# Kernel optimization log

Measured on AMD Instinct MI355X. Metric: run time of the kernel, lower is better.

The kernel has to match this reference:

```python
import jax, jax.numpy as jnp
import numpy as np

B, S, D, H, L = 32, 512, 256, 8, 3
HD = D // H
FFN = D // 2
SCALE_BASE = 512.0
EPS = 1e-5


def _gammas():
    return (1.0 - jnp.exp(jnp.linspace(np.log(1.0 / 32.0), np.log(1.0 / 512.0), H))).astype(jnp.float32)


def _xpos(x, downscale):
    # x: [..., S, hd]; XPOS rotary embedding with exponential length scaling
    s, hd = x.shape[-2], x.shape[-1]
    half = hd // 2
    scale = (jnp.arange(0, hd, 2, dtype=jnp.float32) + 0.4 * hd) / (1.4 * hd)  # [half]
    power = jnp.arange(s, dtype=jnp.float32)[:, None] / SCALE_BASE
    sm = scale[None, :] ** power  # [S, half]
    if downscale:
        sm = 1.0 / sm
    inv_freq = 1.0 / (10000.0 ** (jnp.arange(half, dtype=jnp.float32) / half))
    ang = jnp.arange(s, dtype=jnp.float32)[:, None] * inv_freq[None, :]  # [S, half]
    sin = jnp.repeat(jnp.sin(ang) * sm, 2, axis=-1)  # duplicate_interleave -> [S, hd]
    cos = jnp.repeat(jnp.cos(ang) * sm, 2, axis=-1)
    x1, x2 = x[..., ::2], x[..., 1::2]
    rot = jnp.stack((-x2, x1), axis=-1).reshape(x.shape)  # rotate_every_two
    return x * cos + rot * sin


def _layer_norm(x, w, b):
    mu = x.mean(-1, keepdims=True)
    var = ((x - mu) ** 2).mean(-1, keepdims=True)
    return (x - mu) / jnp.sqrt(var + EPS) * w + b


def _msr(X, WQ, WK, WV, WG, WO, gn_w, gn_b):
    # Multi-scale retention, parallel form. X: [B,S,D]; WQ/WK/WV: [H,D,HD]
    b, s, _ = X.shape
    Q = _xpos(jnp.einsum('bsd,hde->bhse', X, WQ), False)
    K = _xpos(jnp.einsum('bsd,hde->bhse', X, WK), True)
    V = jnp.einsum('bsd,hde->bhse', X, WV)
    n = jnp.arange(s)
    delta = (n[:, None] - n[None, :]).astype(jnp.float32)
    mask = n[:, None] >= n[None, :]
    g = _gammas()
    Dm = jnp.where(mask[None], g[:, None, None] ** delta[None], 0.0)  # [H,S,S]
    scores = jnp.einsum('bhse,bhte->bhst', Q, K) * Dm[None]  # [B,H,S,S]
    Y = jnp.einsum('bhst,bhte->bhse', scores, V)  # [B,H,S,HD]
    Y = jnp.moveaxis(Y, 1, 2)  # [B,S,H,HD] (= concat heads)
    # GroupNorm(heads, v_dim): normalize per (token, head) group
    mu = Y.mean(-1, keepdims=True)
    var = ((Y - mu) ** 2).mean(-1, keepdims=True)
    Yn = ((Y - mu) / jnp.sqrt(var + EPS)).reshape(b, s, D) * gn_w + gn_b
    G = X @ WG
    return (G * jax.nn.sigmoid(G) * Yn) @ WO


def setup_inputs() -> dict:
    key = jax.random.key(0)
    ks = jax.random.split(key, 10)
    inp = {
        'v': jax.random.randint(ks[0], (B, S), 0, 65, dtype=jnp.int64),
        'emb': jax.random.normal(ks[1], (65, D), dtype=jnp.float32),
        'WQ': jax.random.normal(ks[2], (L, H, D, HD), dtype=jnp.float32) / D,
        'WK': jax.random.normal(ks[3], (L, H, D, HD), dtype=jnp.float32) / D,
        'WV': jax.random.normal(ks[4], (L, H, D, HD), dtype=jnp.float32) / D,
        'WG': jax.random.normal(ks[5], (L, D, D), dtype=jnp.float32) / D,
        'WO': jax.random.normal(ks[6], (L, D, D), dtype=jnp.float32) / D,
        'gn_w': jnp.ones((L, D), jnp.float32),
        'gn_b': jnp.zeros((L, D), jnp.float32),
        'ln1_w': jnp.ones((L, D), jnp.float32),
        'ln1_b': jnp.zeros((L, D), jnp.float32),
        'ln2_w': jnp.ones((L, D), jnp.float32),
        'ln2_b': jnp.zeros((L, D), jnp.float32),
        'w1': jax.random.normal(ks[7], (L, D, FFN), dtype=jnp.float32) * (1.0 / np.sqrt(D)),
        'b1': jnp.zeros((L, FFN), jnp.float32),
        'w2': jax.random.normal(ks[8], (L, FFN, D), dtype=jnp.float32) * (1.0 / np.sqrt(FFN)),
        'b2': jnp.zeros((L, D), jnp.float32),
    }
    return inp


def reference(v, emb, WQ, WK, WV, WG, WO, gn_w, gn_b, ln1_w, ln1_b, ln2_w, ln2_b, w1, b1, w2, b2):
    emb = emb.at[0].set(0.0)  # padding_idx=0
    X = jax.nn.relu(emb[v])  # [B,S,D]
    for i in range(L):
        Y = _msr(_layer_norm(X, ln1_w[i], ln1_b[i]), WQ[i], WK[i], WV[i], WG[i], WO[i], gn_w[i], gn_b[i]) + X
        h = jax.nn.gelu(_layer_norm(Y, ln2_w[i], ln2_b[i]) @ w1[i] + b1[i], approximate=False)
        X = h @ w2[i] + b2[i] + Y
    return X
```

## Files before the change

kernel.cpp:

```cpp
#include <hip/hip_runtime.h>
#include <hip/hip_bf16.h>
#include <math.h>

#define BB 32
#define SS 512
#define DD 256
#define HH 8
#define HDIM 32
#define FFNN 128
#define NROWS (BB*SS)
#define NELEM (NROWS*DD)

using bf16 = __hip_bfloat16;
typedef __attribute__((ext_vector_type(8))) short short8;
typedef __attribute__((ext_vector_type(4))) short short4v;
typedef __attribute__((ext_vector_type(4))) float floatx4;
typedef unsigned int uint_al __attribute__((may_alias));

static __device__ __forceinline__ float bf2f(bf16 x) { return __bfloat162float(x); }
static __device__ __forceinline__ bf16  f2bf(float x) { return __float2bfloat16(x); }
static __device__ __forceinline__ short f2bfs(float x) {
    bf16 b = __float2bfloat16(x);
    return __builtin_bit_cast(short, b);
}

static __device__ __forceinline__ unsigned int cvtpk(float a, float b) {
    unsigned int r;
    asm("v_cvt_pk_bf16_f32 %0, %1, %2" : "=v"(r) : "v"(a), "v"(b));
    return r;
}
static __device__ __forceinline__ short4v mk4(unsigned int a, unsigned int b) {
    union { unsigned int u[2]; short4v s; } t;
    t.u[0] = a; t.u[1] = b;
    return t.s;
}
static __device__ __forceinline__ floatx4 mfma16(short4v a, short4v b, floatx4 c) {
#if __has_builtin(__builtin_amdgcn_mfma_f32_16x16x16bf16_1k)
    return __builtin_amdgcn_mfma_f32_16x16x16bf16_1k(a, b, c, 0, 0, 0);
#else
    asm("v_mfma_f32_16x16x16_bf16 %0, %1, %2, %0" : "+v"(c) : "v"(a), "v"(b));
    return c;
#endif
}

static __device__ __forceinline__ void gld_lds16(const void* g, void* l) {
    __builtin_amdgcn_global_load_lds(
        (const __attribute__((address_space(1))) void*)g,
        (__attribute__((address_space(3))) void*)l, 16, 0, 0);
}

__global__ __launch_bounds__(256) void detect_v(const int* __restrict__ v, int* __restrict__ flag) {
    int i = blockIdx.x * 256 + threadIdx.x;
    if (v[2 * i + 1] != 0) atomicOr(flag, 1);
}

#define NQKVG (3*1024*256)
#define NWO   (3*256*256)
#define NW1   (3*128*256)
#define NW2   (3*256*128)
#define NXPT  (512*16)
#define NSETUP (NQKVG+NWO+NW1+NW2+NXPT)
__global__ __launch_bounds__(256) void setup_pack(const float* __restrict__ WQ, const float* __restrict__ WK,
                                                  const float* __restrict__ WV, const float* __restrict__ WG,
                                                  const float* __restrict__ WO, const float* __restrict__ w1,
                                                  const float* __restrict__ w2,
                                                  bf16* __restrict__ dQ, bf16* __restrict__ dO,
                                                  bf16* __restrict__ d1, bf16* __restrict__ d2,
                                                  float4* __restrict__ xpt, int* __restrict__ flag) {
    int idx = blockIdx.x * 256 + threadIdx.x;
    if (idx == 0) *flag = 0;
    if (idx < NQKVG) {
        int k = idx & 255, n = (idx >> 8) & 1023, l = idx >> 18;
        int seg = n >> 8, n8 = n & 255;
        float val;
        if (seg < 3) {
            const float* W = (seg == 0) ? WQ : (seg == 1) ? WK : WV;
            int h = n8 >> 5, e = n8 & 31;
            val = W[(((size_t)l * 8 + h) * 256 + k) * 32 + e];
        } else {
            val = WG[(size_t)l * 65536 + k * 256 + n8];
        }
        dQ[((size_t)l * 1024 + n) * 256 + k] = f2bf(val);
    } else if (idx < NQKVG + NWO) {
        int i = idx - NQKVG;
        int k = i & 255, n = (i >> 8) & 255, l = i >> 16;
        dO[((size_t)l * 256 + n) * 256 + k] = f2bf(WO[(size_t)l * 65536 + k * 256 + n]);
    } else if (idx < NQKVG + NWO + NW1) {
        int i = idx - NQKVG - NWO;
        int k = i & 255, n = (i >> 8) & 127, l = i >> 15;
        d1[((size_t)l * 128 + n) * 256 + k] = f2bf(w1[(size_t)l * 32768 + k * 128 + n]);
    } else if (idx < NQKVG + NWO + NW1 + NW2) {
        int i = idx - NQKVG - NWO - NW1;
        int k = i & 127, n = (i >> 7) & 255, l = i >> 15;
        d2[((size_t)l * 256 + n) * 128 + k] = f2bf(w2[(size_t)l * 32768 + k * 256 + n]);
    } else {
        int i = idx - NQKVG - NWO - NW1 - NW2;
        int jf = i & 15, s = i >> 4;
        float base = (2.0f * jf + 12.8f) / 44.8f;
        float sm = powf(base, (float)s * (1.0f / 512.0f));
        float ang = (float)s * powf(10000.0f, -(float)jf / 16.0f);
        float sn, cs;
        sincosf(ang, &sn, &cs);
        xpt[i] = float4{cs * sm, sn * sm, cs / sm, sn / sm};
    }
}

__global__ __launch_bounds__(256) void embed_ln_kernel(const int* __restrict__ v,
                                                       const float* __restrict__ emb,
                                                       const int* __restrict__ flag,
                                                       const float* __restrict__ w,
                                                       const float* __restrict__ b,
                                                       float* __restrict__ X,
                                                       short* __restrict__ Xn) {
    __shared__ float p1[4], p2[4], st[2];
    const int d = threadIdx.x;
    const int wid = threadIdx.x >> 6;
    const int is32 = *flag;
    const float wd = w[d], bd = b[d];
    for (int it = 0; it < 8; ++it) {
        int row = blockIdx.x * 8 + it;
        int tok = is32 ? v[row] : v[2 * row];
        float x = 0.0f;
        if (tok != 0) {
            x = emb[tok * DD + d];
            x = x > 0.0f ? x : 0.0f;
        }
        X[(size_t)row * DD + d] = x;
        float s1 = x, s2 = x * x;
        #pragma unroll
        for (int off = 1; off < 64; off <<= 1) {
            s1 += __shfl_xor(s1, off);
            s2 += __shfl_xor(s2, off);
        }
        if ((threadIdx.x & 63) == 0) { p1[wid] = s1; p2[wid] = s2; }
        __syncthreads();
        if (threadIdx.x == 0) {
            float t1 = p1[0] + p1[1] + p1[2] + p1[3];
            float t2 = p2[0] + p2[1] + p2[2] + p2[3];
            float mu = t1 * (1.0f / DD);
            float var = t2 * (1.0f / DD) - mu * mu;
            st[0] = mu; st[1] = rsqrtf(var + 1e-5f);
        }
        __syncthreads();
        Xn[(size_t)row * DD + d] = f2bfs((x - st[0]) * st[1] * wd + bd);
    }
}

__global__ __launch_bounds__(256) void qkvg_gemm(const short* __restrict__ A,
                                                 const short* __restrict__ Bp,
                                                 const float4* __restrict__ xpt,
                                                 bf16* __restrict__ C) {
    __shared__ __align__(16) short Als[16 * 512];
    __shared__ __align__(16) short Bls[16 * 512];
    const int tid = threadIdx.x;
    const int wave = tid >> 6, lane = tid & 63, lo = lane & 15, quad = lane >> 4;
    const int wm = wave >> 1, wn = wave & 1;
    const int row0 = blockIdx.x * 128, col0 = blockIdx.y * 128;

    floatx4 acc[4][4];
    #pragma unroll
    for (int i = 0; i < 4; ++i)
        #pragma unroll
        for (int j = 0; j < 4; ++j) acc[i][j] = floatx4{0.f, 0.f, 0.f, 0.f};

    for (int k0 = 0; k0 < 256; k0 += 64) {
        #pragma unroll
        for (int t = 0; t < 4; ++t) {
            int grp = (wm * 4 + t) * 2 + wn;
            const short* ga = A + (size_t)(row0 + (wm * 4 + t) * 16 + lo) * 256
                            + k0 + (wn * 4 + quad) * 8;
            gld_lds16(ga, &Als[grp * 512]);
        }
        #pragma unroll
        for (int t = 0; t < 4; ++t) {
            int grp = (wn * 4 + t) * 2 + wm;
            const short* gb = Bp + (size_t)(col0 + (wn * 4 + t) * 16 + lo) * 256
                            + k0 + (wm * 4 + quad) * 8;
            gld_lds16(gb, &Bls[grp * 512]);
        }
        __syncthreads();
        #pragma unroll
        for (int kkgrp = 0; kkgrp < 2; ++kkgrp) {
            short8 af[4], bfr[4];
            #pragma unroll
            for (int t = 0; t < 4; ++t)
                af[t] = *(const short8*)(&Als[((wm * 4 + t) * 2 + kkgrp) * 512 + lane * 8]);
            #pragma unroll
            for (int t = 0; t < 4; ++t)
                bfr[t] = *(const short8*)(&Bls[((wn * 4 + t) * 2 + kkgrp) * 512 + lane * 8]);
            #pragma unroll
            for (int ti = 0; ti < 4; ++ti)
                #pragma unroll
                for (int tj = 0; tj < 4; ++tj)
                    acc[ti][tj] = __builtin_amdgcn_mfma_f32_16x16x32_bf16(af[ti], bfr[tj], acc[ti][tj], 0, 0, 0);
        }
        __syncthreads();
    }

    #pragma unroll
    for (int ti = 0; ti < 4; ++ti) {
        #pragma unroll
        for (int tj = 0; tj < 4; ++tj) {
            int colb = col0 + (wn * 4 + tj) * 16 + lo;
            int seg = colb >> 8;
            #pragma unroll
            for (int r = 0; r < 4; ++r) {
                int row = row0 + (wm * 4 + ti) * 16 + quad * 4 + r;
                float v = acc[ti][tj][r];
                if (seg < 2) {
                    int s = row & (SS - 1);
                    int jf = (colb & 31) >> 1;
                    float4 t = xpt[s * 16 + jf];
                    float cs = (seg == 0) ? t.x : t.z;
                    float sn = (seg == 0) ? t.y : t.w;
                    float p = __shfl_xor(v, 1);
                    v = (lo & 1) ? (v * cs + p * sn) : (v * cs - p * sn);
                }
                C[(size_t)row * 1024 + colb] = f2bf(v);
            }
        }
    }
}

#define HS2 264
#define HSTR 136
template<int DOLN>
__global__ __launch_bounds__(256) void wo_ffn_fused(const short* __restrict__ A,
                                                    const short* __restrict__ Wo,
                                                    const short* __restrict__ W1p,
                                                    const float* __restrict__ b1,
                                                    const short* __restrict__ W2p,
                                                    const float* __restrict__ b2,
                                                    float* __restrict__ X,
                                                    const float* __restrict__ ln2w,
                                                    const float* __restrict__ ln2b,
                                                    const float* __restrict__ ln1w,
                                                    const float* __restrict__ ln1b,
                                                    short* __restrict__ Xn) {
    __shared__ __align__(16) short Als[4 * 512];
    __shared__ __align__(16) short Bls[4][8 * 512];
    __shared__ __align__(16) short Hn[32 * HS2];
    __shared__ __align__(16) short Hf[32 * HSTR];
    __shared__ float Ssum[32][4], Ssq[32][4];
    const int tid = threadIdx.x;
    const int wave = tid >> 6, lane = tid & 63, lo = lane & 15, quad = lane >> 4;
    const int row0 = blockIdx.x * 32;
    const int colw0 = wave * 64;

    floatx4 acc[2][4];
    #pragma unroll
    for (int i = 0; i < 2; ++i)
        #pragma unroll
        for (int j = 0; j < 4; ++j) acc[i][j] = floatx4{0.f, 0.f, 0.f, 0.f};

    const short* Ab = A + (size_t)(row0 + (wave >> 1) * 16 + lo) * 1024 + ((wave & 1) * 4 + quad) * 8;
    const short* Bb = Wo + (size_t)(colw0 + lo) * 256 + quad * 8;

    for (int k0 = 0; k0 < 256; k0 += 64) {
        gld_lds16(Ab + k0, &Als[wave * 512]);
        #pragma unroll
        for (int t = 0; t < 4; ++t)
            #pragma unroll
            for (int kk = 0; kk < 2; ++kk)
                gld_lds16(Bb + (size_t)(t * 16) * 256 + k0 + kk * 32,
                          &Bls[wave][(t * 2 + kk) * 512]);
        __syncthreads();
        #pragma unroll
        for (int kk = 0; kk < 2; ++kk) {
            short8 af[2], bfr[4];
            #pragma unroll
            for (int t = 0; t < 2; ++t)
                af[t] = *(const short8*)(&Als[(t * 2 + kk) * 512 + lane * 8]);
            #pragma unroll
            for (int t = 0; t < 4; ++t)
                bfr[t] = *(const short8*)(&Bls[wave][(t * 2 + kk) * 512 + lane * 8]);
            #pragma unroll
            for (int ti = 0; ti < 2; ++ti)
                #pragma unroll
                for (int tj = 0; tj < 4; ++tj)
                    acc[ti][tj] = __builtin_amdgcn_mfma_f32_16x16x32_bf16(af[ti], bfr[tj], acc[ti][tj], 0, 0, 0);
        }
        __syncthreads();
    }

    float vv[2][4][4];
    #pragma unroll
    for (int ti = 0; ti < 2; ++ti)
        #pragma unroll
        for (int tj = 0; tj < 4; ++tj) {
            int colb = colw0 + tj * 16 + lo;
            #pragma unroll
            for (int r = 0; r < 4; ++r) {
                int row = row0 + ti * 16 + quad * 4 + r;
                vv[ti][tj][r] = acc[ti][tj][r] + X[(size_t)row * DD + colb];
            }
        }
    #pragma unroll
    for (int ti = 0; ti < 2; ++ti)
        #pragma unroll
        for (int r = 0; r < 4; ++r) {
            float s1 = 0.f, s2 = 0.f;
            #pragma unroll
            for (int tj = 0; tj < 4; ++tj) {
                float v = vv[ti][tj][r];
                s1 += v; s2 += v * v;
            }
            #pragma unroll
            for (int off = 1; off < 16; off <<= 1) {
                s1 += __shfl_xor(s1, off);
                s2 += __shfl_xor(s2, off);
            }
            if (lo == 0) {
                int rl = ti * 16 + quad * 4 + r;
                Ssum[rl][wave] = s1;
                Ssq[rl][wave] = s2;
            }
        }
    __syncthreads();
    #pragma unroll
    for (int ti = 0; ti < 2; ++ti)
        #pragma unroll
        for (int r = 0; r < 4; ++r) {
            int rl = ti * 16 + quad * 4 + r;
            float t1 = Ssum[rl][0] + Ssum[rl][1] + Ssum[rl][2] + Ssum[rl][3];
            float t2 = Ssq[rl][0] + Ssq[rl][1] + Ssq[rl][2] + Ssq[rl][3];
            float mu = t1 * (1.0f / DD);
            float var = t2 * (1.0f / DD) - mu * mu;
            float rs = rsqrtf(var + 1e-5f);
            #pragma unroll
            for (int tj = 0; tj < 4; ++tj) {
                int colb = colw0 + tj * 16 + lo;
                Hn[rl * HS2 + colb] =
                    f2bfs((vv[ti][tj][r] - mu) * rs * ln2w[colb] + ln2b[colb]);
            }
        }
    __syncthreads();

    floatx4 a1[2][2];
    #pragma unroll
    for (int i = 0; i < 2; ++i) { a1[i][0] = floatx4{0,0,0,0}; a1[i][1] = floatx4{0,0,0,0}; }
    const short* Bb1 = W1p + (size_t)(wave * 32 + lo) * 256 + quad * 8;
    for (int k0 = 0; k0 < 256; k0 += 64) {
        #pragma unroll
        for (int t = 0; t < 2; ++t)
            #pragma unroll
            for (int kk = 0; kk < 2; ++kk)
                gld_lds16(Bb1 + (size_t)(t * 16) * 256 + k0 + kk * 32,
                          &Bls[wave][(t * 2 + kk) * 512]);
        __syncthreads();
        #pragma unroll
        for (int kk = 0; kk < 2; ++kk) {
            short8 af[2], bfr[2];
            #pragma unroll
            for (int t = 0; t < 2; ++t)
                af[t] = *(const short8*)(&Hn[(t * 16 + lo) * HS2 + k0 + kk * 32 + quad * 8]);
            #pragma unroll
            for (int t = 0; t < 2; ++t)
                bfr[t] = *(const short8*)(&Bls[wave][(t * 2 + kk) * 512 + lane * 8]);
            #pragma unroll
            for (int ti = 0; ti < 2; ++ti)
                #pragma unroll
                for (int tj = 0; tj < 2; ++tj)
                    a1[ti][tj] = __builtin_amdgcn_mfma_f32_16x16x32_bf16(af[ti], bfr[tj], a1[ti][tj], 0, 0, 0);
        }
        __syncthreads();
    }
    #pragma unroll
    for (int ti = 0; ti < 2; ++ti)
        #pragma unroll
        for (int tj = 0; tj < 2; ++tj) {
            int colb = wave * 32 + tj * 16 + lo;
            float bs = b1[colb];
            #pragma unroll
            for (int r = 0; r < 4; ++r) {
                int rl = ti * 16 + quad * 4 + r;
                float v = a1[ti][tj][r] + bs;
                v = 0.5f * v * (1.0f + erff(v * 0.70710678118f));
                Hf[rl * HSTR + colb] = f2bfs(v);
            }
        }

    floatx4 a2[2][4];
    #pragma unroll
    for (int i = 0; i < 2; ++i)
        #pragma unroll
        for (int j = 0; j < 4; ++j) a2[i][j] = floatx4{0,0,0,0};
    const short* Bb2 = W2p + (size_t)(colw0 + lo) * 128 + quad * 8;
    for (int k0 = 0; k0 < 128; k0 += 64) {
        #pragma unroll
        for (int t = 0; t < 4; ++t)
            #pragma unroll
            for (int kk = 0; kk < 2; ++kk)
                gld_lds16(Bb2 + (size_t)(t * 16) * 128 + k0 + kk * 32,
                          &Bls[wave][(t * 2 + kk) * 512]);
        __syncthreads();
        #pragma unroll
        for (int kk = 0; kk < 2; ++kk) {
            short8 af[2], bfr[4];
            #pragma unroll
            for (int t = 0; t < 2; ++t)
                af[t] = *(const short8*)(&Hf[(t * 16 + lo) * HSTR + k0 + kk * 32 + quad * 8]);
            #pragma unroll
            for (int t = 0; t < 4; ++t)
                bfr[t] = *(const short8*)(&Bls[wave][(t * 2 + kk) * 512 + lane * 8]);
            #pragma unroll
            for (int ti = 0; ti < 2; ++ti)
                #pragma unroll
                for (int tj = 0; tj < 4; ++tj)
                    a2[ti][tj] = __builtin_amdgcn_mfma_f32_16x16x32_bf16(af[ti], bfr[tj], a2[ti][tj], 0, 0, 0);
        }
        __syncthreads();
    }

    #pragma unroll
    for (int ti = 0; ti < 2; ++ti)
        #pragma unroll
        for (int tj = 0; tj < 4; ++tj) {
            int colb = colw0 + tj * 16 + lo;
            float bs = b2[colb];
            #pragma unroll
            for (int r = 0; r < 4; ++r) {
                int row = row0 + ti * 16 + quad * 4 + r;
                float v = a2[ti][tj][r] + bs + vv[ti][tj][r];
                X[(size_t)row * DD + colb] = v;
                vv[ti][tj][r] = v;
            }
        }
    if (!DOLN) return;
    #pragma unroll
    for (int ti = 0; ti < 2; ++ti)
        #pragma unroll
        for (int r = 0; r < 4; ++r) {
            float s1 = 0.f, s2 = 0.f;
            #pragma unroll
            for (int tj = 0; tj < 4; ++tj) {
                float v = vv[ti][tj][r];
                s1 += v; s2 += v * v;
            }
            #pragma unroll
            for (int off = 1; off < 16; off <<= 1) {
                s1 += __shfl_xor(s1, off);
                s2 += __shfl_xor(s2, off);
            }
            if (lo == 0) {
                int rl = ti * 16 + quad * 4 + r;
                Ssum[rl][wave] = s1;
                Ssq[rl][wave] = s2;
            }
        }
    __syncthreads();
    #pragma unroll
    for (int ti = 0; ti < 2; ++ti)
        #pragma unroll
        for (int r = 0; r < 4; ++r) {
            int rl = ti * 16 + quad * 4 + r;
            float t1 = Ssum[rl][0] + Ssum[rl][1] + Ssum[rl][2] + Ssum[rl][3];
            float t2 = Ssq[rl][0] + Ssq[rl][1] + Ssq[rl][2] + Ssq[rl][3];
            float mu = t1 * (1.0f / DD);
            float var = t2 * (1.0f / DD) - mu * mu;
            float rs = rsqrtf(var + 1e-5f);
            int row = row0 + rl;
            #pragma unroll
            for (int tj = 0; tj < 4; ++tj) {
                int colb = colw0 + tj * 16 + lo;
                Xn[(size_t)row * DD + colb] =
                    f2bfs((vv[ti][tj][r] - mu) * rs * ln1w[colb] + ln1b[colb]);
            }
        }
}

#define VSTR 44
__global__ __launch_bounds__(256) void retention_mfma_kernel(bf16* __restrict__ QKVG,
                                                             const float* __restrict__ gnw,
                                                             const float* __restrict__ gnb) {
    __shared__ __align__(16) short Vt[4][32 * VSTR];
    const int wslot = threadIdx.x >> 6;
    const int lane = threadIdx.x & 63;
    const int gblk = blockIdx.x >> 6;
    const int qi = 15 - ((gblk & ~3) + (((gblk & 3) + (gblk >> 2)) & 3));
    const int bh = ((blockIdx.x & 63) << 2) | wslot;
    const int b = bh >> 3, h = bh & 7;
    const int q0 = qi * 32;
    const int lo = lane & 15, quad = lane >> 4;

    const float la0 = -3.46573590280f, la1 = -6.23832462504f;
    float gamma = 1.0f - expf(la0 + (float)h * (la1 - la0) / 7.0f);
    float lg2 = log2f(gamma);
    float g16i = exp2f(-16.0f * lg2);
    float g16p = exp2f(16.0f * lg2);
    float gi32 = exp2f(-32.0f * lg2);
    float wq[4], wq16[4], wqB[4];
    #pragma unroll
    for (int r = 0; r < 4; ++r) {
        wq[r]   = exp2f((float)(lo - 4 * quad - r) * lg2);
        wq16[r] = wq[r] * g16i;
        wqB[r]  = wq[r] * g16p;
    }
    float c = exp2f((float)q0 * lg2);

    const size_t base = (size_t)b * SS * 1024;
    const short* QKVGs = (const short*)QKVG;

    short8 qfA = *(const short8*)(QKVGs + base + (size_t)(q0 + lo) * 1024 + h * HDIM + quad * 8);
    short8 qfB = *(const short8*)(QKVGs + base + (size_t)(q0 + 16 + lo) * 1024 + h * HDIM + quad * 8);

    floatx4 oA0 = {0,0,0,0}, oA1 = {0,0,0,0}, oB0 = {0,0,0,0}, oB1 = {0,0,0,0};
    short* Vw = Vt[wslot];
    const int nch = qi + 1;

    for (int ch = 0; ch < nch; ++ch) {
        const int t0 = ch * 32;
        const short* Kb = QKVGs + base + 256 + h * HDIM + quad * 8;
        short8 kf0 = *(const short8*)(Kb + (size_t)(t0 + lo) * 1024);
        short8 kf1 = *(const short8*)(Kb + (size_t)(t0 + 16 + lo) * 1024);
        {
            const int r = lane >> 2, dcol = (lane & 3) * 8;
            const short* Vg = QKVGs + base + 512 + h * HDIM + dcol;
            uint4 u1 = *(const uint4*)(Vg + (size_t)(t0 + r) * 1024);
            uint4 u2 = *(const uint4*)(Vg + (size_t)(t0 + 16 + r) * 1024);
            uint_al* W1 = (uint_al*)(Vw + r * VSTR + dcol);
            uint_al* W2 = (uint_al*)(Vw + (16 + r) * VSTR + dcol);
            W1[0] = u1.x; W1[1] = u1.y; W1[2] = u1.z; W1[3] = u1.w;
            W2[0] = u2.x; W2[1] = u2.y; W2[2] = u2.z; W2[3] = u2.w;
        }
        const floatx4 z = {0,0,0,0};
        __builtin_amdgcn_s_setprio(1);
        floatx4 sA0 = __builtin_amdgcn_mfma_f32_16x16x32_bf16(kf0, qfA, z, 0, 0, 0);
        floatx4 sA1 = __builtin_amdgcn_mfma_f32_16x16x32_bf16(kf1, qfA, z, 0, 0, 0);
        floatx4 sB0 = __builtin_amdgcn_mfma_f32_16x16x32_bf16(kf0, qfB, z, 0, 0, 0);
        floatx4 sB1 = __builtin_amdgcn_mfma_f32_16x16x32_bf16(kf1, qfB, z, 0, 0, 0);
        __builtin_amdgcn_s_setprio(0);

        float m0[4], m1[4], mB[4];
        #pragma unroll
        for (int r = 0; r < 4; ++r) {
            m0[r] = c * wq[r];
            m1[r] = c * wq16[r];
            mB[r] = c * wqB[r];
        }
        if (ch == qi) {
            #pragma unroll
            for (int r = 0; r < 4; ++r) {
                if (lo < 4 * quad + r) m0[r] = 0.0f;
                m1[r] = 0.0f;
            }
        }
        c *= gi32;

        unsigned int pa0 = cvtpk(sA0[0] * m0[0], sA0[1] * m0[1]);
        unsigned int pa1 = cvtpk(sA0[2] * m0[2], sA0[3] * m0[3]);
        unsigned int pa2 = cvtpk(sA1[0] * m1[0], sA1[1] * m1[1]);
        unsigned int pa3 = cvtpk(sA1[2] * m1[2], sA1[3] * m1[3]);
        unsigned int pb0 = cvtpk(sB0[0] * mB[0], sB0[1] * mB[1]);
        unsigned int pb1 = cvtpk(sB0[2] * mB[2], sB0[3] * mB[3]);
        unsigned int pb2 = cvtpk(sB1[0] * m0[0], sB1[1] * m0[1]);
        unsigned int pb3 = cvtpk(sB1[2] * m0[2], sB1[3] * m0[3]);
        short4v pA0 = mk4(pa0, pa1), pA1 = mk4(pa2, pa3);
        short4v pB0 = mk4(pb0, pb1), pB1 = mk4(pb2, pb3);

        short4v v00, v01, v10, v11;
        #pragma unroll
        for (int j = 0; j < 4; ++j) {
            v00[j] = Vw[(4 * quad + j) * VSTR + lo];
            v01[j] = Vw[(16 + 4 * quad + j) * VSTR + lo];
            v10[j] = Vw[(4 * quad + j) * VSTR + 16 + lo];
            v11[j] = Vw[(16 + 4 * quad + j) * VSTR + 16 + lo];
        }
        __builtin_amdgcn_s_setprio(1);
        oA0 = mfma16(pA0, v00, oA0);
        oA0 = mfma16(pA1, v01, oA0);
        oA1 = mfma16(pA0, v10, oA1);
        oA1 = mfma16(pA1, v11, oA1);
        oB0 = mfma16(pB0, v00, oB0);
        oB0 = mfma16(pB1, v01, oB0);
        oB1 = mfma16(pB0, v10, oB1);
        oB1 = mfma16(pB1, v11, oB1);
        __builtin_amdgcn_s_setprio(0);
    }

    float gw0 = gnw[h * HDIM + lo], gw1 = gnw[h * HDIM + 16 + lo];
    float gb0 = gnb[h * HDIM + lo], gb1 = gnb[h * HDIM + 16 + lo];
    bf16* QK = QKVG;
    #pragma unroll
    for (int sub = 0; sub < 2; ++sub) {
        floatx4 o0 = sub ? oB0 : oA0;
        floatx4 o1 = sub ? oB1 : oA1;
        int qbase = q0 + sub * 16;
        #pragma unroll
        for (int r = 0; r < 4; ++r) {
            float y0 = o0[r], y1 = o1[r];
            float s = y0 + y1, ss = y0 * y0 + y1 * y1;
            #pragma unroll
            for (int off = 1; off < 16; off <<= 1) {
                s  += __shfl_xor(s, off);
                ss += __shfl_xor(ss, off);
            }
            float mu = s * (1.0f / HDIM);
            float var = ss * (1.0f / HDIM) - mu * mu;
            float rstd = rsqrtf(var + 1e-5f);
            int q = qbase + quad * 4 + r;
            size_t rowb = base + (size_t)q * 1024;
            float g0 = bf2f(QK[rowb + 768 + h * HDIM + lo]);
            float g1 = bf2f(QK[rowb + 768 + h * HDIM + 16 + lo]);
            float t0v = g0 / (1.0f + expf(-g0)) * ((y0 - mu) * rstd * gw0 + gb0);
            float t1v = g1 / (1.0f + expf(-g1)) * ((y1 - mu) * rstd * gw1 + gb1);
            QK[rowb + h * HDIM + lo]      = f2bf(t0v);
            QK[rowb + h * HDIM + 16 + lo] = f2bf(t1v);
        }
    }
}

extern "C" void kernel_launch(void* const* d_in, const int* in_sizes, int n_in,
                              void* d_out, int out_size, void* d_ws, size_t ws_size,
                              hipStream_t stream) {
    const int*   v    = (const int*)d_in[0];
    const float* emb  = (const float*)d_in[1];
    const float* WQ   = (const float*)d_in[2];
    const float* WK   = (const float*)d_in[3];
    const float* WV   = (const float*)d_in[4];
    const float* WG   = (const float*)d_in[5];
    const float* WO   = (const float*)d_in[6];
    const float* gn_w = (const float*)d_in[7];
    const float* gn_b = (const float*)d_in[8];
    const float* ln1w = (const float*)d_in[9];
    const float* ln1b = (const float*)d_in[10];
    const float* ln2w = (const float*)d_in[11];
    const float* ln2b = (const float*)d_in[12];
    const float* w1   = (const float*)d_in[13];
    const float* b1   = (const float*)d_in[14];
    const float* w2   = (const float*)d_in[15];
    const float* b2   = (const float*)d_in[16];

    float* X = (float*)d_out;

    float* base  = (float*)d_ws;
    int*   flag  = (int*)base;
    short* Xn    = (short*)(base + 16);
    bf16*  QKVG  = (bf16*)(Xn + (size_t)NROWS * 256);
    bf16*  WqkvgP = QKVG + (size_t)NROWS * 1024;
    bf16*  WoP   = WqkvgP + 3 * 1024 * 256;
    bf16*  W1P   = WoP + 3 * 256 * 256;
    bf16*  W2P   = W1P + 3 * 128 * 256;
    float4* xpt  = (float4*)(W2P + 3 * 256 * 128);

    setup_pack<<<NSETUP / 256, 256, 0, stream>>>(WQ, WK, WV, WG, WO, w1, w2,
                                                 WqkvgP, WoP, W1P, W2P, xpt, flag);
    detect_v<<<32, 256, 0, stream>>>(v, flag);
    embed_ln_kernel<<<NROWS / 8, 256, 0, stream>>>(v, emb, flag, ln1w, ln1b, X, Xn);

    for (int i = 0; i < 3; ++i) {
        qkvg_gemm<<<dim3(128, 8), 256, 0, stream>>>(Xn,
                                                    (const short*)(WqkvgP + (size_t)i * 1024 * 256),
                                                    xpt, QKVG);
        retention_mfma_kernel<<<1024, 256, 0, stream>>>(QKVG, gn_w + i * DD, gn_b + i * DD);
        if (i < 2)
            wo_ffn_fused<1><<<NROWS / 32, 256, 0, stream>>>((const short*)QKVG,
                                                            (const short*)(WoP + (size_t)i * 256 * 256),
                                                            (const short*)(W1P + (size_t)i * 128 * 256),
                                                            b1 + i * FFNN,
                                                            (const short*)(W2P + (size_t)i * 256 * 128),
                                                            b2 + i * DD, X,
                                                            ln2w + i * DD, ln2b + i * DD,
                                                            ln1w + (i + 1) * DD, ln1b + (i + 1) * DD, Xn);
        else
            wo_ffn_fused<0><<<NROWS / 32, 256, 0, stream>>>((const short*)QKVG,
                                                            (const short*)(WoP + (size_t)i * 256 * 256),
                                                            (const short*)(W1P + (size_t)i * 128 * 256),
                                                            b1 + i * FFNN,
                                                            (const short*)(W2P + (size_t)i * 256 * 128),
                                                            b2 + i * DD, X,
                                                            ln2w + i * DD, ln2b + i * DD,
                                                            nullptr, nullptr, nullptr);
    }
}
```

Measured before the change: 352.4 us.

## Load MFMA operands directly from global memory instead of staging through LDS

```diff
diff --git a/kernel.cpp b/kernel.cpp
--- a/kernel.cpp
+++ b/kernel.cpp
@@ -237,8 +237,6 @@
                                                     const float* __restrict__ ln1w,
                                                     const float* __restrict__ ln1b,
                                                     short* __restrict__ Xn) {
-    __shared__ __align__(16) short Als[4 * 512];
-    __shared__ __align__(16) short Bls[4][8 * 512];
     __shared__ __align__(16) short Hn[32 * HS2];
     __shared__ __align__(16) short Hf[32 * HSTR];
     __shared__ float Ssum[32][4], Ssq[32][4];
@@ -246,6 +244,7 @@
     const int wave = tid >> 6, lane = tid & 63, lo = lane & 15, quad = lane >> 4;
     const int row0 = blockIdx.x * 32;
     const int colw0 = wave * 64;
+    const int kq = quad * 8;
 
     floatx4 acc[2][4];
     #pragma unroll
@@ -253,34 +252,23 @@
         #pragma unroll
         for (int j = 0; j < 4; ++j) acc[i][j] = floatx4{0.f, 0.f, 0.f, 0.f};
 
-    const short* Ab = A + (size_t)(row0 + (wave >> 1) * 16 + lo) * 1024 + ((wave & 1) * 4 + quad) * 8;
-    const short* Bb = Wo + (size_t)(colw0 + lo) * 256 + quad * 8;
-
     for (int k0 = 0; k0 < 256; k0 += 64) {
-        gld_lds16(Ab + k0, &Als[wave * 512]);
-        #pragma unroll
-        for (int t = 0; t < 4; ++t)
-            #pragma unroll
-            for (int kk = 0; kk < 2; ++kk)
-                gld_lds16(Bb + (size_t)(t * 16) * 256 + k0 + kk * 32,
-                          &Bls[wave][(t * 2 + kk) * 512]);
-        __syncthreads();
         #pragma unroll
         for (int kk = 0; kk < 2; ++kk) {
+            const int kof = k0 + kk * 32 + kq;
             short8 af[2], bfr[4];
             #pragma unroll
             for (int t = 0; t < 2; ++t)
-                af[t] = *(const short8*)(&Als[(t * 2 + kk) * 512 + lane * 8]);
+                af[t] = *(const short8*)(A + (size_t)(row0 + t * 16 + lo) * 1024 + kof);
             #pragma unroll
             for (int t = 0; t < 4; ++t)
-                bfr[t] = *(const short8*)(&Bls[wave][(t * 2 + kk) * 512 + lane * 8]);
+                bfr[t] = *(const short8*)(Wo + (size_t)(colw0 + t * 16 + lo) * 256 + kof);
             #pragma unroll
             for (int ti = 0; ti < 2; ++ti)
                 #pragma unroll
                 for (int tj = 0; tj < 4; ++tj)
                     acc[ti][tj] = __builtin_amdgcn_mfma_f32_16x16x32_bf16(af[ti], bfr[tj], acc[ti][tj], 0, 0, 0);
         }
-        __syncthreads();
     }
 
     float vv[2][4][4];
@@ -339,31 +327,23 @@
     floatx4 a1[2][2];
     #pragma unroll
     for (int i = 0; i < 2; ++i) { a1[i][0] = floatx4{0,0,0,0}; a1[i][1] = floatx4{0,0,0,0}; }
-    const short* Bb1 = W1p + (size_t)(wave * 32 + lo) * 256 + quad * 8;
     for (int k0 = 0; k0 < 256; k0 += 64) {
         #pragma unroll
-        for (int t = 0; t < 2; ++t)
-            #pragma unroll
-            for (int kk = 0; kk < 2; ++kk)
-                gld_lds16(Bb1 + (size_t)(t * 16) * 256 + k0 + kk * 32,
-                          &Bls[wave][(t * 2 + kk) * 512]);
-        __syncthreads();
-        #pragma unroll
         for (int kk = 0; kk < 2; ++kk) {
+            const int kof = k0 + kk * 32 + kq;
             short8 af[2], bfr[2];
             #pragma unroll
             for (int t = 0; t < 2; ++t)
-                af[t] = *(const short8*)(&Hn[(t * 16 + lo) * HS2 + k0 + kk * 32 + quad * 8]);
+                af[t] = *(const short8*)(&Hn[(t * 16 + lo) * HS2 + kof]);
             #pragma unroll
             for (int t = 0; t < 2; ++t)
-                bfr[t] = *(const short8*)(&Bls[wave][(t * 2 + kk) * 512 + lane * 8]);
+                bfr[t] = *(const short8*)(W1p + (size_t)(wave * 32 + t * 16 + lo) * 256 + kof);
             #pragma unroll
             for (int ti = 0; ti < 2; ++ti)
                 #pragma unroll
                 for (int tj = 0; tj < 2; ++tj)
                     a1[ti][tj] = __builtin_amdgcn_mfma_f32_16x16x32_bf16(af[ti], bfr[tj], a1[ti][tj], 0, 0, 0);
         }
-        __syncthreads();
     }
     #pragma unroll
     for (int ti = 0; ti < 2; ++ti)
@@ -379,37 +359,30 @@
                 Hf[rl * HSTR + colb] = f2bfs(v);
             }
         }
+    __syncthreads();
 
     floatx4 a2[2][4];
     #pragma unroll
     for (int i = 0; i < 2; ++i)
         #pragma unroll
         for (int j = 0; j < 4; ++j) a2[i][j] = floatx4{0,0,0,0};
-    const short* Bb2 = W2p + (size_t)(colw0 + lo) * 128 + quad * 8;
     for (int k0 = 0; k0 < 128; k0 += 64) {
         #pragma unroll
-        for (int t = 0; t < 4; ++t)
-            #pragma unroll
-            for (int kk = 0; kk < 2; ++kk)
-                gld_lds16(Bb2 + (size_t)(t * 16) * 128 + k0 + kk * 32,
-                          &Bls[wave][(t * 2 + kk) * 512]);
-        __syncthreads();
-        #pragma unroll
         for (int kk = 0; kk < 2; ++kk) {
+            const int kof = k0 + kk * 32 + kq;
             short8 af[2], bfr[4];
             #pragma unroll
             for (int t = 0; t < 2; ++t)
-                af[t] = *(const short8*)(&Hf[(t * 16 + lo) * HSTR + k0 + kk * 32 + quad * 8]);
+                af[t] = *(const short8*)(&Hf[(t * 16 + lo) * HSTR + kof]);
             #pragma unroll
             for (int t = 0; t < 4; ++t)
-                bfr[t] = *(const short8*)(&Bls[wave][(t * 2 + kk) * 512 + lane * 8]);
+                bfr[t] = *(const short8*)(W2p + (size_t)(colw0 + t * 16 + lo) * 128 + kof);
             #pragma unroll
             for (int ti = 0; ti < 2; ++ti)
                 #pragma unroll
                 for (int tj = 0; tj < 4; ++tj)
                     a2[ti][tj] = __builtin_amdgcn_mfma_f32_16x16x32_bf16(af[ti], bfr[tj], a2[ti][tj], 0, 0, 0);
         }
-        __syncthreads();
     }
 
     #pragma unroll
```

Result: no change. 352.1 us (-0.1%).
